# Kernel tuning notes

Hardware: AMD Instinct MI355X
Metric: run time of the kernel (lower is better)

The kernel has to match this reference:

```python
import jax, jax.numpy as jnp
import numpy as np

N = 50000  # nodes


def gcn_layer(x, src, dst, W, b):
    """DGL GraphConv with norm='both': D_in^{-1/2} A^T D_out^{-1/2} x W + b."""
    E = src.shape[0]
    ones = jnp.ones((E,), dtype=x.dtype)
    deg_out = jax.ops.segment_sum(ones, src, num_segments=N)  # out-degree of src nodes
    deg_in = jax.ops.segment_sum(ones, dst, num_segments=N)   # in-degree of dst nodes
    norm_src = jax.lax.rsqrt(jnp.maximum(deg_out, 1.0))
    norm_dst = jax.lax.rsqrt(jnp.maximum(deg_in, 1.0))
    h = x * norm_src[:, None]
    agg = jax.ops.segment_sum(h[src], dst, num_segments=N)  # [N, in_dim]
    return (agg @ W) * norm_dst[:, None] + b


def encoder(feat, src, dst, W1, b1, W2, b2):
    h = jax.nn.relu(gcn_layer(feat, src, dst, W1, b1))
    h = jax.nn.relu(gcn_layer(h, src, dst, W2, b2))
    return h


def proj(h, fc1_W, fc1_b, fc2_W, fc2_b):
    z = jax.nn.elu(h @ fc1_W + fc1_b)
    return z @ fc2_W + fc2_b


def setup_inputs() -> dict:
    key = jax.random.key(0)
    ks = jax.random.split(key, 12)
    in_dim, hid, out_dim, E = 128, 128, 128, 800000
    inp = {
        "feat1": jax.random.normal(ks[0], (N, in_dim), dtype=jnp.float32),
        "feat2": jax.random.normal(ks[1], (N, in_dim), dtype=jnp.float32),
        "edge_index1": jax.random.randint(ks[2], (2, E), 0, N),
        "edge_index2": jax.random.randint(ks[3], (2, E), 0, N),
        # GraphConv weights: in_dim -> 2*hid -> hid
        "conv1_W": jax.random.normal(ks[4], (in_dim, 2 * hid), dtype=jnp.float32) * 0.05,
        "conv1_b": jnp.zeros((2 * hid,), dtype=jnp.float32),
        "conv2_W": jax.random.normal(ks[5], (2 * hid, hid), dtype=jnp.float32) * 0.05,
        "conv2_b": jnp.zeros((hid,), dtype=jnp.float32),
        # MLP proj: fc1 hid->out, fc2 out->hid
        "fc1_W": jax.random.normal(ks[6], (hid, out_dim), dtype=jnp.float32) * 0.05,
        "fc1_b": jnp.zeros((out_dim,), dtype=jnp.float32),
        "fc2_W": jax.random.normal(ks[7], (out_dim, hid), dtype=jnp.float32) * 0.05,
        "fc2_b": jnp.zeros((hid,), dtype=jnp.float32),
    }
    return inp


def reference(feat1, feat2, edge_index1, edge_index2,
              conv1_W, conv1_b, conv2_W, conv2_b,
              fc1_W, fc1_b, fc2_W, fc2_b):
    h1 = encoder(feat1, edge_index1[0], edge_index1[1], conv1_W, conv1_b, conv2_W, conv2_b)
    h2 = encoder(feat2, edge_index2[0], edge_index2[1], conv1_W, conv1_b, conv2_W, conv2_b)
    z1 = proj(h1, fc1_W, fc1_b, fc2_W, fc2_b)
    z2 = proj(h2, fc1_W, fc1_b, fc2_W, fc2_b)
    return (z1, z2)
```

## Files before the change

### kernel.cpp

```cpp
#include <hip/hip_runtime.h>
#include <math.h>

#define NDIM 128
#define H2   256
#define MAXG 2
#define TPE  8192
#define NBKMAX 512

typedef __attribute__((ext_vector_type(8))) short bf16x8;
typedef __attribute__((ext_vector_type(4))) float f32x4;

__device__ __forceinline__ unsigned short f2bf(float f) {
    unsigned int u = __float_as_uint(f);
    u += 0x7fffu + ((u >> 16) & 1u);
    return (unsigned short)(u >> 16);
}
__device__ __forceinline__ float bf2f(unsigned short h) {
    return __uint_as_float(((unsigned int)h) << 16);
}
__device__ __forceinline__ void split2(float f, unsigned short& h, unsigned short& l) {
    h = f2bf(f);
    l = f2bf(f - bf2f(h));
}

struct BinArgs {
    const int* src[MAXG]; const int* dst[MAXG];
    int* histD[MAXG]; int* histS[MAXG];
    int* totD[MAXG];  int* baseD[MAXG];
    int* totS[MAXG];  int* baseS[MAXG];
    unsigned int* pairs[MAXG];
    unsigned short* srcS[MAXG];
    int E[MAXG]; int NBK; int NT; int n;
};

__global__ __launch_bounds__(256) void binA(BinArgs a) {
    __shared__ int cntD[NBKMAX], cntS[NBKMAX];
    int g = blockIdx.y, t = blockIdx.x, tid = threadIdx.x;
    for (int b = tid; b < NBKMAX; b += 256) { cntD[b] = 0; cntS[b] = 0; }
    __syncthreads();
    int E = a.E[g];
    int base = t * TPE;
#pragma unroll
    for (int k = 0; k < TPE / 256; ++k) {
        int e = base + k * 256 + tid;
        if (e < E) {
            atomicAdd(&cntD[a.dst[g][e] >> 7], 1);
            atomicAdd(&cntS[a.src[g][e] >> 7], 1);
        }
    }
    __syncthreads();
    for (int b = tid; b < a.NBK; b += 256) {
        a.histD[g][t * a.NBK + b] = cntD[b];
        a.histS[g][t * a.NBK + b] = cntS[b];
    }
}

__global__ __launch_bounds__(512) void binB(BinArgs a) {
    int g = blockIdx.y, side = blockIdx.z;
    int* hist = side ? a.histS[g] : a.histD[g];
    int* tot  = side ? a.totS[g]  : a.totD[g];
    int* base = side ? a.baseS[g] : a.baseD[g];
    __shared__ int s[512];
    int b = threadIdx.x;
    int v = 0;
    if (b < a.NBK)
        for (int t = 0; t < a.NT; ++t) v += hist[t * a.NBK + b];
    s[b] = v;
    __syncthreads();
    for (int off = 1; off < 512; off <<= 1) {
        int u = (b >= off) ? s[b - off] : 0;
        __syncthreads();
        s[b] += u;
        __syncthreads();
    }
    int excl = s[b] - v;
    if (b < a.NBK) {
        tot[b] = v;
        base[b] = excl;
        int run = excl;
        for (int t = 0; t < a.NT; ++t) {
            int h = hist[t * a.NBK + b];
            hist[t * a.NBK + b] = run;
            run += h;
        }
    }
}

__global__ __launch_bounds__(256) void binC(BinArgs a) {
    __shared__ int offD[NBKMAX], offS[NBKMAX];
    int g = blockIdx.y, t = blockIdx.x, tid = threadIdx.x;
    for (int b = tid; b < a.NBK; b += 256) {
        offD[b] = a.histD[g][t * a.NBK + b];
        offS[b] = a.histS[g][t * a.NBK + b];
    }
    __syncthreads();
    int E = a.E[g];
    int base = t * TPE;
    unsigned int* pairs = a.pairs[g];
    unsigned short* ss = a.srcS[g];
#pragma unroll
    for (int k = 0; k < TPE / 256; ++k) {
        int e = base + k * 256 + tid;
        if (e < E) {
            int s = a.src[g][e], d = a.dst[g][e];
            int pos = atomicAdd(&offD[d >> 7], 1);
            pairs[pos] = ((unsigned int)(d & 127) << 16) | (unsigned int)s;
            int posS = atomicAdd(&offS[s >> 7], 1);
            ss[posS] = (unsigned short)s;
        }
    }
}

struct FinArgs {
    const unsigned int* pairs[MAXG];
    const unsigned short* srcS[MAXG];
    const int* totD[MAXG]; const int* baseD[MAXG];
    const int* totS[MAXG]; const int* baseS[MAXG];
    int* row_ptr[MAXG]; int* row_end[MAXG];
    unsigned short* edge_srt[MAXG];
    float* ns[MAXG]; float* nd[MAXG];
    int n;
};

__global__ __launch_bounds__(256) void finalize(FinArgs a) {
    __shared__ int cnt[128], hist[128], scn[128], cur[128];
    int g = blockIdx.y, bkt = blockIdx.x, tid = threadIdx.x;
    if (tid < 128) { cnt[tid] = 0; hist[tid] = 0; }
    __syncthreads();
    {
        int base = a.baseS[g][bkt], tot = a.totS[g][bkt];
        const unsigned short* ss = a.srcS[g];
        for (int i = tid; i < tot; i += 256)
            atomicAdd(&cnt[ss[base + i] & 127], 1);
    }
    int cntE = a.totD[g][bkt], base = a.baseD[g][bkt];
    const unsigned int* pp = a.pairs[g] + base;
    for (int i = tid; i < cntE; i += 256)
        atomicAdd(&hist[pp[i] >> 16], 1);
    __syncthreads();
    if (tid < 128) {
        int node = bkt * 128 + tid;
        if (node < a.n) {
            int c = cnt[tid];
            a.ns[g][node] = rsqrtf((float)(c > 1 ? c : 1));
        }
        scn[tid] = hist[tid];
    }
    __syncthreads();
    for (int off = 1; off < 128; off <<= 1) {
        int v = (tid < 128 && tid >= off) ? scn[tid - off] : 0;
        __syncthreads();
        if (tid < 128) scn[tid] += v;
        __syncthreads();
    }
    if (tid < 128) {
        int incl = scn[tid];
        int h = hist[tid];
        cur[tid] = incl - h;
        int node = bkt * 128 + tid;
        if (node < a.n) {
            a.row_ptr[g][node] = base + incl - h;
            a.row_end[g][node] = base + incl;
            a.nd[g][node] = rsqrtf((float)(h > 1 ? h : 1));
        }
    }
    __syncthreads();
    for (int i = tid; i < cntE; i += 256) {
        unsigned int p = pp[i];
        int pos = atomicAdd(&cur[p >> 16], 1);
        a.edge_srt[g][base + pos] = (unsigned short)(p & 0xFFFF);
    }
}

__global__ void wprep_all(const float* __restrict__ W1, const float* __restrict__ W2,
                          const float* __restrict__ F1, const float* __restrict__ F2,
                          unsigned short* __restrict__ W1h, unsigned short* __restrict__ W1l,
                          unsigned short* __restrict__ W2h, unsigned short* __restrict__ W2l,
                          unsigned short* __restrict__ F1h, unsigned short* __restrict__ F1l,
                          unsigned short* __restrict__ F2h, unsigned short* __restrict__ F2l) {
    int i = blockIdx.x * 256 + threadIdx.x;
    const float* Wsrc; unsigned short *Hd, *Ld; int K, Nc, idx;
    if (i < 32768)       { Wsrc = W1; Hd = W1h; Ld = W1l; K = 128; Nc = 256; idx = i; }
    else if (i < 65536)  { Wsrc = W2; Hd = W2h; Ld = W2l; K = 256; Nc = 128; idx = i - 32768; }
    else if (i < 81920)  { Wsrc = F1; Hd = F1h; Ld = F1l; K = 128; Nc = 128; idx = i - 65536; }
    else                 { Wsrc = F2; Hd = F2h; Ld = F2l; K = 128; Nc = 128; idx = i - 81920; }
    int k = idx / Nc, n = idx % Nc;
    unsigned short h, l;
    split2(Wsrc[idx], h, l);
    Hd[n * K + k] = h;
    Ld[n * K + k] = l;
}

struct FusedArgs {
    const float* Xg[MAXG];
    const int* rp[MAXG]; const int* re[MAXG];
    const unsigned short* ep[MAXG];
    const float* sns[MAXG];
    const float* ndv[MAXG];
    const float* gbias;
    const unsigned short* B1h; const unsigned short* B1l;
    const unsigned short* B2h; const unsigned short* B2l;
    const float* rs1[MAXG]; const float* rs2[MAXG];
    const float* b1v; const float* b2v;
    float* C[MAXG];
    int M, has_rs1, has_rs2, has_b1, has_b2;
};

template <int K1, int N1, int ACT1, int ROWS, int GMODE>
__global__ __launch_bounds__(512, 8) void fused_g(FusedArgs a) {
    constexpr int IR   = ROWS / 16;
    constexpr int SH_A = ROWS * K1;
    constexpr int SH_X = ROWS * N1;
    constexpr int SH   = (2 * SH_A > 2 * SH_X) ? 2 * SH_A : 2 * SH_X;
    __shared__ __align__(16) unsigned short S[SH];
    unsigned short* As_h = S;
    unsigned short* As_l = S + SH_A;
    unsigned short* Xs_h = S;
    unsigned short* Xs_l = S + SH_X;

    int g = blockIdx.y;
    const unsigned short* __restrict__ B1h = a.B1h;
    const unsigned short* __restrict__ B1l = a.B1l;
    const unsigned short* __restrict__ B2h = a.B2h;
    const unsigned short* __restrict__ B2l = a.B2l;

    int tid  = threadIdx.x;
    int wave = tid >> 6, lane = tid & 63;
    int quad = lane >> 4, l16 = lane & 15;
    int rowBase = blockIdx.x * ROWS;
    int M = a.M;

    {
        int half  = tid >> 5;
        int glane = tid & 31;
        const float* X   = a.Xg[g];
        const float* sns = a.sns[g];
        const unsigned short* ep = a.ep[g];
        int base = glane * 4;
#pragma unroll
        for (int ps = 0; ps < ROWS / 16; ++ps) {
            int row  = ps * 16 + half;
            int grow = rowBase + row;
            float4 acc = make_float4(0.f, 0.f, 0.f, 0.f);
            if (grow < M) {
                int j = a.rp[g][grow], end = a.re[g][grow];
                if (GMODE == 1) {
                    for (; j + 3 < end; j += 4) {
                        int s0 = ep[j], s1 = ep[j + 1], s2 = ep[j + 2], s3 = ep[j + 3];
                        float n0 = sns[s0], n1 = sns[s1], n2 = sns[s2], n3 = sns[s3];
                        float4 v0 = *(const float4*)(X + (size_t)s0 * NDIM + base);
                        float4 v1 = *(const float4*)(X + (size_t)s1 * NDIM + base);
                        float4 v2 = *(const float4*)(X + (size_t)s2 * NDIM + base);
                        float4 v3 = *(const float4*)(X + (size_t)s3 * NDIM + base);
                        acc.x = fmaf(v0.x, n0, fmaf(v1.x, n1, fmaf(v2.x, n2, fmaf(v3.x, n3, acc.x))));
                        acc.y = fmaf(v0.y, n0, fmaf(v1.y, n1, fmaf(v2.y, n2, fmaf(v3.y, n3, acc.y))));
                        acc.z = fmaf(v0.z, n0, fmaf(v1.z, n1, fmaf(v2.z, n2, fmaf(v3.z, n3, acc.z))));
                        acc.w = fmaf(v0.w, n0, fmaf(v1.w, n1, fmaf(v2.w, n2, fmaf(v3.w, n3, acc.w))));
                    }
                    for (; j < end; ++j) {
                        int s0 = ep[j];
                        float n0 = sns[s0];
                        float4 v0 = *(const float4*)(X + (size_t)s0 * NDIM + base);
                        acc.x = fmaf(v0.x, n0, acc.x); acc.y = fmaf(v0.y, n0, acc.y);
                        acc.z = fmaf(v0.z, n0, acc.z); acc.w = fmaf(v0.w, n0, acc.w);
                    }
                } else {
                    for (; j + 3 < end; j += 4) {
                        int s0 = ep[j], s1 = ep[j + 1], s2 = ep[j + 2], s3 = ep[j + 3];
                        float4 v0 = *(const float4*)(X + (size_t)s0 * NDIM + base);
                        float4 v1 = *(const float4*)(X + (size_t)s1 * NDIM + base);
                        float4 v2 = *(const float4*)(X + (size_t)s2 * NDIM + base);
                        float4 v3 = *(const float4*)(X + (size_t)s3 * NDIM + base);
                        acc.x += v0.x + v1.x + v2.x + v3.x;
                        acc.y += v0.y + v1.y + v2.y + v3.y;
                        acc.z += v0.z + v1.z + v2.z + v3.z;
                        acc.w += v0.w + v1.w + v2.w + v3.w;
                    }
                    for (; j < end; ++j) {
                        int s0 = ep[j];
                        float4 v0 = *(const float4*)(X + (size_t)s0 * NDIM + base);
                        acc.x += v0.x; acc.y += v0.y; acc.z += v0.z; acc.w += v0.w;
                    }
                }
            }
            float v[4] = {acc.x, acc.y, acc.z, acc.w};
            if (GMODE == 2) {
                float s = (grow < M) ? a.ndv[g][grow] : 0.f;
#pragma unroll
                for (int c = 0; c < 4; ++c)
                    v[c] = fmaxf(v[c] * s + a.gbias[base + c], 0.f);
            }
            unsigned short h[4], l[4];
#pragma unroll
            for (int c = 0; c < 4; ++c) split2(v[c], h[c], l[c]);
            int oc = glane >> 1, within = (glane & 1) * 4;
            int sc = oc ^ (row & 7);
            *(ushort4*)(As_h + row * K1 + sc * 8 + within) = make_ushort4(h[0], h[1], h[2], h[3]);
            *(ushort4*)(As_l + row * K1 + sc * 8 + within) = make_ushort4(l[0], l[1], l[2], l[3]);
        }
    }

    constexpr int J1  = (N1 / 128 > 0) ? N1 / 128 : 1;
    constexpr int KT1 = K1 / 32;
    constexpr int KT2 = N1 / 32;
    int wcol1 = wave * (N1 / 8);
    int wcol2 = wave * 16;

    size_t b1off[J1];
#pragma unroll
    for (int j = 0; j < J1; ++j)
        b1off[j] = (size_t)(wcol1 + j * 16 + l16) * K1 + quad * 8;
    size_t b2off = (size_t)(wcol2 + l16) * N1 + quad * 8;

    auto loadB1 = [&](int kt, bf16x8 (&bh)[J1], bf16x8 (&bl)[J1]) {
#pragma unroll
        for (int j = 0; j < J1; ++j) {
            bh[j] = *(const bf16x8*)(B1h + b1off[j] + kt * 32);
            bl[j] = *(const bf16x8*)(B1l + b1off[j] + kt * 32);
        }
    };
    auto loadB2 = [&](int kt, bf16x8 (&bh)[1], bf16x8 (&bl)[1]) {
        bh[0] = *(const bf16x8*)(B2h + b2off + kt * 32);
        bl[0] = *(const bf16x8*)(B2l + b2off + kt * 32);
    };

    bf16x8 b1hA[J1], b1lA[J1], b1hB[J1], b1lB[J1];
    loadB1(0, b1hA, b1lA);
    __syncthreads();

    f32x4 acc1[IR][J1] = {};
    auto stepP1 = [&](int kt, bf16x8 (&bh)[J1], bf16x8 (&bl)[J1]) {
        bf16x8 af[IR], alf[IR];
#pragma unroll
        for (int i = 0; i < IR; ++i) {
            int r  = i * 16 + l16;
            int sc = (kt * 4 + quad) ^ (r & 7);
            af[i]  = *(const bf16x8*)(As_h + r * K1 + sc * 8);
            alf[i] = *(const bf16x8*)(As_l + r * K1 + sc * 8);
        }
#pragma unroll
        for (int i = 0; i < IR; ++i)
#pragma unroll
            for (int j = 0; j < J1; ++j) {
                acc1[i][j] = __builtin_amdgcn_mfma_f32_16x16x32_bf16(af[i],  bh[j], acc1[i][j], 0, 0, 0);
                acc1[i][j] = __builtin_amdgcn_mfma_f32_16x16x32_bf16(alf[i], bh[j], acc1[i][j], 0, 0, 0);
                acc1[i][j] = __builtin_amdgcn_mfma_f32_16x16x32_bf16(af[i],  bl[j], acc1[i][j], 0, 0, 0);
            }
    };
#pragma unroll
    for (int kt = 0; kt < KT1; kt += 2) {
        if (kt + 1 < KT1) loadB1(kt + 1, b1hB, b1lB);
        stepP1(kt, b1hA, b1lA);
        if (kt + 2 < KT1) loadB1(kt + 2, b1hA, b1lA);
        if (kt + 1 < KT1) stepP1(kt + 1, b1hB, b1lB);
    }

    bf16x8 b2hA[1], b2lA[1], b2hB[1], b2lB[1];
    loadB2(0, b2hA, b2lA);

    __syncthreads();

    const float* rs1p = a.has_rs1 ? a.rs1[g] : nullptr;
#pragma unroll
    for (int i = 0; i < IR; ++i) {
#pragma unroll
        for (int rr = 0; rr < 4; ++rr) {
            int row  = i * 16 + quad * 4 + rr;
            int grow = rowBase + row;
            float rs = 1.0f;
            if (rs1p) rs = (grow < M) ? rs1p[grow] : 0.0f;
#pragma unroll
            for (int j = 0; j < J1; ++j) {
                int col = wcol1 + j * 16 + l16;
                float v = acc1[i][j][rr] * rs;
                if (a.has_b1) v += a.b1v[col];
                if (ACT1 == 1) v = fmaxf(v, 0.f);
                else           v = v > 0.f ? v : expm1f(v);
                unsigned short h, l;
                split2(v, h, l);
                int oc = col >> 3, within = col & 7;
                int sc = oc ^ (row & 7);
                Xs_h[row * N1 + sc * 8 + within] = h;
                Xs_l[row * N1 + sc * 8 + within] = l;
            }
        }
    }
    __syncthreads();

    f32x4 acc2[IR][1] = {};
    auto stepP2 = [&](int kt, bf16x8 (&bh)[1], bf16x8 (&bl)[1]) {
        bf16x8 xf[IR], xlf[IR];
#pragma unroll
        for (int i = 0; i < IR; ++i) {
            int r  = i * 16 + l16;
            int sc = (kt * 4 + quad) ^ (r & 7);
            xf[i]  = *(const bf16x8*)(Xs_h + r * N1 + sc * 8);
            xlf[i] = *(const bf16x8*)(Xs_l + r * N1 + sc * 8);
        }
#pragma unroll
        for (int i = 0; i < IR; ++i) {
            acc2[i][0] = __builtin_amdgcn_mfma_f32_16x16x32_bf16(xf[i],  bh[0], acc2[i][0], 0, 0, 0);
            acc2[i][0] = __builtin_amdgcn_mfma_f32_16x16x32_bf16(xlf[i], bh[0], acc2[i][0], 0, 0, 0);
            acc2[i][0] = __builtin_amdgcn_mfma_f32_16x16x32_bf16(xf[i],  bl[0], acc2[i][0], 0, 0, 0);
        }
    };
#pragma unroll
    for (int kt = 0; kt < KT2; kt += 2) {
        if (kt + 1 < KT2) loadB2(kt + 1, b2hB, b2lB);
        stepP2(kt, b2hA, b2lA);
        if (kt + 2 < KT2) loadB2(kt + 2, b2hA, b2lA);
        if (kt + 1 < KT2) stepP2(kt + 1, b2hB, b2lB);
    }

    const float* rs2p = a.has_rs2 ? a.rs2[g] : nullptr;
#pragma unroll
    for (int i = 0; i < IR; ++i) {
#pragma unroll
        for (int rr = 0; rr < 4; ++rr) {
            int grow = rowBase + i * 16 + quad * 4 + rr;
            if (grow >= M) continue;
            float rs = rs2p ? rs2p[grow] : 1.0f;
            int col = wcol2 + l16;
            float v = acc2[i][0][rr] * rs;
            if (a.has_b2) v += a.b2v[col];
            a.C[g][(size_t)grow * NDIM + col] = v;
        }
    }
}

extern "C" void kernel_launch(void* const* d_in, const int* in_sizes, int n_in,
                              void* d_out, int out_size, void* d_ws, size_t ws_size,
                              hipStream_t stream) {
    const float* feat[2] = {(const float*)d_in[0], (const float*)d_in[1]};
    const int*   ei[2]   = {(const int*)d_in[2], (const int*)d_in[3]};
    const float* W1   = (const float*)d_in[4];
    const float* b1   = (const float*)d_in[5];
    const float* W2   = (const float*)d_in[6];
    const float* b2   = (const float*)d_in[7];
    const float* fc1W = (const float*)d_in[8];
    const float* fc1b = (const float*)d_in[9];
    const float* fc2W = (const float*)d_in[10];
    const float* fc2b = (const float*)d_in[11];
    int N = in_sizes[0] / NDIM;
    float* out = (float*)d_out;

    int Emax = 0;
    for (int g = 0; g < 2; ++g) { int E = in_sizes[2 + g] / 2; if (E > Emax) Emax = E; }
    int NBK = (N + 127) / 128;
    int NT  = (Emax + TPE - 1) / TPE;

    char* p = (char*)d_ws;
    float* ns_[2]; float* nd_[2];
    for (int i = 0; i < 2; ++i) { ns_[i] = (float*)p; p += (size_t)N * 4; }
    for (int i = 0; i < 2; ++i) { nd_[i] = (float*)p; p += (size_t)N * 4; }
    int* rp_[2]; int* re_[2]; unsigned short* esrt_[2];
    for (int i = 0; i < 2; ++i) { rp_[i] = (int*)p; p += (size_t)N * 4; }
    for (int i = 0; i < 2; ++i) { re_[i] = (int*)p; p += (size_t)N * 4; }
    for (int i = 0; i < 2; ++i) { esrt_[i] = (unsigned short*)p; p += (size_t)Emax * 2; }
    unsigned short* R1[2]; unsigned short* R2[2];
    for (int i = 0; i < 2; ++i) { R1[i] = (unsigned short*)p; p += (size_t)N * NDIM * 2 * 2; }
    for (int i = 0; i < 2; ++i) { R2[i] = (unsigned short*)p; p += (size_t)N * H2 * 2 * 2; }
    unsigned short* W1th = (unsigned short*)p; p += (size_t)NDIM * H2 * 2;
    unsigned short* W1tl = (unsigned short*)p; p += (size_t)NDIM * H2 * 2;
    unsigned short* W2th = (unsigned short*)p; p += (size_t)H2 * NDIM * 2;
    unsigned short* W2tl = (unsigned short*)p; p += (size_t)H2 * NDIM * 2;
    unsigned short* f1th = (unsigned short*)p; p += (size_t)NDIM * NDIM * 2;
    unsigned short* f1tl = (unsigned short*)p; p += (size_t)NDIM * NDIM * 2;
    unsigned short* f2th = (unsigned short*)p; p += (size_t)NDIM * NDIM * 2;
    unsigned short* f2tl = (unsigned short*)p; p += (size_t)NDIM * NDIM * 2;
    int* tb = (int*)p; p += (size_t)2 * 4 * NBK * 4;

    int* histD_[2]; int* histS_[2]; unsigned int* pairs_[2]; unsigned short* srcS_[2];
    for (int i = 0; i < 2; ++i) {
        histD_[i] = (int*)R2[i];
        histS_[i] = (int*)R2[i] + (size_t)NT * NBK;
        pairs_[i] = (unsigned int*)((char*)R2[i] + (1 << 20));
        srcS_[i]  = (unsigned short*)R1[i];
    }

    BinArgs ba = {};
    ba.NBK = NBK; ba.NT = NT; ba.n = N;
    for (int i = 0; i < 2; ++i) {
        int E = in_sizes[2 + i] / 2;
        ba.src[i] = ei[i]; ba.dst[i] = ei[i] + E; ba.E[i] = E;
        ba.histD[i] = histD_[i]; ba.histS[i] = histS_[i];
        ba.totD[i]  = tb + (size_t)i * 4 * NBK;
        ba.baseD[i] = tb + (size_t)i * 4 * NBK + NBK;
        ba.totS[i]  = tb + (size_t)i * 4 * NBK + 2 * NBK;
        ba.baseS[i] = tb + (size_t)i * 4 * NBK + 3 * NBK;
        ba.pairs[i] = pairs_[i]; ba.srcS[i] = srcS_[i];
    }

    wprep_all<<<384, 256, 0, stream>>>(W1, W2, fc1W, fc2W,
                                       W1th, W1tl, W2th, W2tl, f1th, f1tl, f2th, f2tl);
    binA<<<dim3(NT, 2), 256, 0, stream>>>(ba);
    binB<<<dim3(1, 2, 2), 512, 0, stream>>>(ba);
    binC<<<dim3(NT, 2), 256, 0, stream>>>(ba);

    FinArgs fa = {};
    fa.n = N;
    for (int i = 0; i < 2; ++i) {
        fa.pairs[i] = pairs_[i]; fa.srcS[i] = srcS_[i];
        fa.totD[i] = ba.totD[i]; fa.baseD[i] = ba.baseD[i];
        fa.totS[i] = ba.totS[i]; fa.baseS[i] = ba.baseS[i];
        fa.row_ptr[i] = rp_[i]; fa.row_end[i] = re_[i];
        fa.edge_srt[i] = esrt_[i];
        fa.ns[i] = ns_[i]; fa.nd[i] = nd_[i];
    }
    finalize<<<dim3(NBK, 2), 256, 0, stream>>>(fa);

    float* T[2];
    for (int i = 0; i < 2; ++i)
        T[i] = (float*)R2[i];

    int mgrid32 = (N + 31) / 32;

    FusedArgs f12 = {};
    f12.B1h = W1th; f12.B1l = W1tl; f12.B2h = W2th; f12.B2l = W2tl;
    f12.b1v = b1; f12.has_b1 = 1; f12.has_b2 = 0;
    f12.has_rs1 = 1; f12.has_rs2 = 1;
    f12.M = N;
    for (int i = 0; i < 2; ++i) {
        f12.Xg[i] = feat[i];
        f12.rp[i] = rp_[i]; f12.re[i] = re_[i]; f12.ep[i] = esrt_[i];
        f12.sns[i] = ns_[i]; f12.ndv[i] = nd_[i];
        f12.rs1[i] = nd_[i]; f12.rs2[i] = ns_[i];
        f12.C[i] = T[i];
    }
    fused_g<128, 256, 1, 32, 1><<<dim3(mgrid32, 2), 512, 0, stream>>>(f12);

    FusedArgs f34 = {};
    f34.B1h = f1th; f34.B1l = f1tl; f34.B2h = f2th; f34.B2l = f2tl;
    f34.b1v = fc1b; f34.has_b1 = 1; f34.b2v = fc2b; f34.has_b2 = 1;
    f34.has_rs1 = 0; f34.has_rs2 = 0;
    f34.gbias = b2;
    f34.M = N;
    for (int i = 0; i < 2; ++i) {
        f34.Xg[i] = T[i];
        f34.rp[i] = rp_[i]; f34.re[i] = re_[i]; f34.ep[i] = esrt_[i];
        f34.sns[i] = ns_[i]; f34.ndv[i] = nd_[i];
        f34.C[i] = out + (size_t)i * N * NDIM;
    }
    fused_g<128, 128, 2, 32, 2><<<dim3(mgrid32, 2), 512, 0, stream>>>(f34);
}
```

Before: 557.3 us.

## Fold weight prep into binning kernel and software-pipeline gather loads

The standalone weight-splitting kernel is merged into binA as extra blocks (WXB per graph slice), saving one launch and letting the weight conversion run concurrently with the edge histogram work. Separately, the neighbor gather loops in the fused aggregation kernel are software-pipelined: the next four rows are loaded before the previous four are accumulated, to hide gather latency. The pipelining raises register pressure, which could lower occupancy.

```diff
diff --git a/kernel.cpp b/kernel.cpp
--- a/kernel.cpp
+++ b/kernel.cpp
@@ -6,6 +6,7 @@
 #define MAXG 2
 #define TPE  8192
 #define NBKMAX 512
+#define WXB  192
 
 typedef __attribute__((ext_vector_type(8))) short bf16x8;
 typedef __attribute__((ext_vector_type(4))) float f32x4;
@@ -33,9 +34,29 @@
     int E[MAXG]; int NBK; int NT; int n;
 };
 
-__global__ __launch_bounds__(256) void binA(BinArgs a) {
+struct WPArgs {
+    const float* src[4];
+    unsigned short* Hd[4]; unsigned short* Ld[4];
+};
+
+__global__ __launch_bounds__(256) void binA(BinArgs a, WPArgs w) {
+    int t = blockIdx.x, tid = threadIdx.x;
+    if (t >= a.NT) {
+        int i = (blockIdx.y * WXB + (t - a.NT)) * 256 + tid;
+        const float* Wsrc; unsigned short *Hd, *Ld; int K, Nc, idx;
+        if (i < 32768)       { Wsrc = w.src[0]; Hd = w.Hd[0]; Ld = w.Ld[0]; K = 128; Nc = 256; idx = i; }
+        else if (i < 65536)  { Wsrc = w.src[1]; Hd = w.Hd[1]; Ld = w.Ld[1]; K = 256; Nc = 128; idx = i - 32768; }
+        else if (i < 81920)  { Wsrc = w.src[2]; Hd = w.Hd[2]; Ld = w.Ld[2]; K = 128; Nc = 128; idx = i - 65536; }
+        else                 { Wsrc = w.src[3]; Hd = w.Hd[3]; Ld = w.Ld[3]; K = 128; Nc = 128; idx = i - 81920; }
+        int k = idx / Nc, n = idx % Nc;
+        unsigned short h, l;
+        split2(Wsrc[idx], h, l);
+        Hd[n * K + k] = h;
+        Ld[n * K + k] = l;
+        return;
+    }
     __shared__ int cntD[NBKMAX], cntS[NBKMAX];
-    int g = blockIdx.y, t = blockIdx.x, tid = threadIdx.x;
+    int g = blockIdx.y;
     for (int b = tid; b < NBKMAX; b += 256) { cntD[b] = 0; cntS[b] = 0; }
     __syncthreads();
     int E = a.E[g];
@@ -170,25 +191,6 @@
         int pos = atomicAdd(&cur[p >> 16], 1);
         a.edge_srt[g][base + pos] = (unsigned short)(p & 0xFFFF);
     }
-}
-
-__global__ void wprep_all(const float* __restrict__ W1, const float* __restrict__ W2,
-                          const float* __restrict__ F1, const float* __restrict__ F2,
-                          unsigned short* __restrict__ W1h, unsigned short* __restrict__ W1l,
-                          unsigned short* __restrict__ W2h, unsigned short* __restrict__ W2l,
-                          unsigned short* __restrict__ F1h, unsigned short* __restrict__ F1l,
-                          unsigned short* __restrict__ F2h, unsigned short* __restrict__ F2l) {
-    int i = blockIdx.x * 256 + threadIdx.x;
-    const float* Wsrc; unsigned short *Hd, *Ld; int K, Nc, idx;
-    if (i < 32768)       { Wsrc = W1; Hd = W1h; Ld = W1l; K = 128; Nc = 256; idx = i; }
-    else if (i < 65536)  { Wsrc = W2; Hd = W2h; Ld = W2l; K = 256; Nc = 128; idx = i - 32768; }
-    else if (i < 81920)  { Wsrc = F1; Hd = F1h; Ld = F1l; K = 128; Nc = 128; idx = i - 65536; }
-    else                 { Wsrc = F2; Hd = F2h; Ld = F2l; K = 128; Nc = 128; idx = i - 81920; }
-    int k = idx / Nc, n = idx % Nc;
-    unsigned short h, l;
-    split2(Wsrc[idx], h, l);
-    Hd[n * K + k] = h;
-    Ld[n * K + k] = l;
 }
 
 struct FusedArgs {
@@ -245,13 +247,28 @@
             if (grow < M) {
                 int j = a.rp[g][grow], end = a.re[g][grow];
                 if (GMODE == 1) {
-                    for (; j + 3 < end; j += 4) {
+                    if (j + 3 < end) {
                         int s0 = ep[j], s1 = ep[j + 1], s2 = ep[j + 2], s3 = ep[j + 3];
                         float n0 = sns[s0], n1 = sns[s1], n2 = sns[s2], n3 = sns[s3];
                         float4 v0 = *(const float4*)(X + (size_t)s0 * NDIM + base);
                         float4 v1 = *(const float4*)(X + (size_t)s1 * NDIM + base);
                         float4 v2 = *(const float4*)(X + (size_t)s2 * NDIM + base);
                         float4 v3 = *(const float4*)(X + (size_t)s3 * NDIM + base);
+                        j += 4;
+                        for (; j + 3 < end; j += 4) {
+                            int t0 = ep[j], t1 = ep[j + 1], t2 = ep[j + 2], t3 = ep[j + 3];
+                            float m0 = sns[t0], m1 = sns[t1], m2 = sns[t2], m3 = sns[t3];
+                            float4 w0 = *(const float4*)(X + (size_t)t0 * NDIM + base);
+                            float4 w1 = *(const float4*)(X + (size_t)t1 * NDIM + base);
+                            float4 w2 = *(const float4*)(X + (size_t)t2 * NDIM + base);
+                            float4 w3 = *(const float4*)(X + (size_t)t3 * NDIM + base);
+                            acc.x = fmaf(v0.x, n0, fmaf(v1.x, n1, fmaf(v2.x, n2, fmaf(v3.x, n3, acc.x))));
+                            acc.y = fmaf(v0.y, n0, fmaf(v1.y, n1, fmaf(v2.y, n2, fmaf(v3.y, n3, acc.y))));
+                            acc.z = fmaf(v0.z, n0, fmaf(v1.z, n1, fmaf(v2.z, n2, fmaf(v3.z, n3, acc.z))));
+                            acc.w = fmaf(v0.w, n0, fmaf(v1.w, n1, fmaf(v2.w, n2, fmaf(v3.w, n3, acc.w))));
+                            v0 = w0; v1 = w1; v2 = w2; v3 = w3;
+                            n0 = m0; n1 = m1; n2 = m2; n3 = m3;
+                        }
                         acc.x = fmaf(v0.x, n0, fmaf(v1.x, n1, fmaf(v2.x, n2, fmaf(v3.x, n3, acc.x))));
                         acc.y = fmaf(v0.y, n0, fmaf(v1.y, n1, fmaf(v2.y, n2, fmaf(v3.y, n3, acc.y))));
                         acc.z = fmaf(v0.z, n0, fmaf(v1.z, n1, fmaf(v2.z, n2, fmaf(v3.z, n3, acc.z))));
@@ -265,12 +282,25 @@
                         acc.z = fmaf(v0.z, n0, acc.z); acc.w = fmaf(v0.w, n0, acc.w);
                     }
                 } else {
-                    for (; j + 3 < end; j += 4) {
+                    if (j + 3 < end) {
                         int s0 = ep[j], s1 = ep[j + 1], s2 = ep[j + 2], s3 = ep[j + 3];
                         float4 v0 = *(const float4*)(X + (size_t)s0 * NDIM + base);
                         float4 v1 = *(const float4*)(X + (size_t)s1 * NDIM + base);
                         float4 v2 = *(const float4*)(X + (size_t)s2 * NDIM + base);
                         float4 v3 = *(const float4*)(X + (size_t)s3 * NDIM + base);
+                        j += 4;
+                        for (; j + 3 < end; j += 4) {
+                            int t0 = ep[j], t1 = ep[j + 1], t2 = ep[j + 2], t3 = ep[j + 3];
+                            float4 w0 = *(const float4*)(X + (size_t)t0 * NDIM + base);
+                            float4 w1 = *(const float4*)(X + (size_t)t1 * NDIM + base);
+                            float4 w2 = *(const float4*)(X + (size_t)t2 * NDIM + base);
+                            float4 w3 = *(const float4*)(X + (size_t)t3 * NDIM + base);
+                            acc.x += v0.x + v1.x + v2.x + v3.x;
+                            acc.y += v0.y + v1.y + v2.y + v3.y;
+                            acc.z += v0.z + v1.z + v2.z + v3.z;
+                            acc.w += v0.w + v1.w + v2.w + v3.w;
+                            v0 = w0; v1 = w1; v2 = w2; v3 = w3;
+                        }
                         acc.x += v0.x + v1.x + v2.x + v3.x;
                         acc.y += v0.y + v1.y + v2.y + v3.y;
                         acc.z += v0.z + v1.z + v2.z + v3.z;
@@ -491,9 +521,13 @@
         ba.pairs[i] = pairs_[i]; ba.srcS[i] = srcS_[i];
     }
 
-    wprep_all<<<384, 256, 0, stream>>>(W1, W2, fc1W, fc2W,
-                                       W1th, W1tl, W2th, W2tl, f1th, f1tl, f2th, f2tl);
-    binA<<<dim3(NT, 2), 256, 0, stream>>>(ba);
+    WPArgs wp = {};
+    wp.src[0] = W1;   wp.Hd[0] = W1th; wp.Ld[0] = W1tl;
+    wp.src[1] = W2;   wp.Hd[1] = W2th; wp.Ld[1] = W2tl;
+    wp.src[2] = fc1W; wp.Hd[2] = f1th; wp.Ld[2] = f1tl;
+    wp.src[3] = fc2W; wp.Hd[3] = f2th; wp.Ld[3] = f2tl;
+
+    binA<<<dim3(NT + WXB, 2), 256, 0, stream>>>(ba, wp);
     binB<<<dim3(1, 2, 2), 512, 0, stream>>>(ba);
     binC<<<dim3(NT, 2), 256, 0, stream>>>(ba);
 
```

After: 553.7 us. About the same (-0.6%).
